# Optimization experiments

Hardware: AMD Instinct MI355X
Metric: run time of the kernel (lower is better)

## Reference

```python
import jax, jax.numpy as jnp
import numpy as np

B, S, D, H = 8, 2048, 1024, 8
HD = D // H


def _linear_params(key, d_in, d_out):
    kw, kb = jax.random.split(key)
    w = jax.random.normal(kw, (d_out, d_in), jnp.float32) * 0.02
    b = jax.random.normal(kb, (d_out,), jnp.float32) * 0.02
    return w, b


def setup_inputs() -> dict:
    key = jax.random.key(0)
    ks = jax.random.split(key, 16)
    inp = {}
    inp['input_seq'] = jax.random.normal(ks[0], (B, S, D), jnp.float32)
    inp['output_seq'] = jax.random.normal(ks[1], (B, S, D), jnp.float32)
    # PositionalEncoding parameter: sin(arange(D) / 10000 ** (arange(D)/D))
    ar = jnp.arange(D, dtype=jnp.float32)
    inp['pe'] = jnp.sin(ar / 10000.0 ** (ar / D))
    names = ['enc_wq enc_bq', 'enc_wk enc_bk', 'enc_wv enc_bv',
             'enc_w1 enc_b1', 'enc_w2 enc_b2',
             'dec_s_wq dec_s_bq', 'dec_s_wk dec_s_bk', 'dec_s_wv dec_s_bv',
             'dec_c_wq dec_c_bq', 'dec_c_wk dec_c_bk', 'dec_c_wv dec_c_bv',
             'dec_w1 dec_b1', 'dec_w2 dec_b2', 'fc_w fc_b']
    for i, pair in enumerate(names):
        wn, bn = pair.split()
        w, b = _linear_params(ks[2 + i], D, D)
        inp[wn], inp[bn] = w, b
    return inp


def _mha(q_in, k_in, wq, bq, wk, bk, wv, bv):
    # Faithful to source: head split WITHOUT transpose -> per-position 8x8 head mixing.
    q = (q_in @ wq.T + bq).reshape(q_in.shape[0], q_in.shape[1], H, HD)
    k = (k_in @ wk.T + bk).reshape(k_in.shape[0], k_in.shape[1], H, HD)
    v = (k_in @ wv.T + bv).reshape(k_in.shape[0], k_in.shape[1], H, HD)
    scores = jnp.einsum('bsih,bsjh->bsij', q, k) / jnp.sqrt(jnp.float32(HD))
    w = jax.nn.softmax(scores, axis=-1)  # dropout before softmax is identity at eval
    out = jnp.einsum('bsij,bsjh->bsih', w, v)
    return out.reshape(q_in.shape[0], q_in.shape[1], -1)


def reference(input_seq, output_seq, pe,
              enc_wq, enc_bq, enc_wk, enc_bk, enc_wv, enc_bv,
              enc_w1, enc_b1, enc_w2, enc_b2,
              dec_s_wq, dec_s_bq, dec_s_wk, dec_s_bk, dec_s_wv, dec_s_bv,
              dec_c_wq, dec_c_bq, dec_c_wk, dec_c_bk, dec_c_wv, dec_c_bv,
              dec_w1, dec_b1, dec_w2, dec_b2, fc_w, fc_b):
    x = input_seq + pe  # additive positional encoding
    # encoder layer
    a = _mha(x, x, enc_wq, enc_bq, enc_wk, enc_bk, enc_wv, enc_bv)
    enc_out = jax.nn.relu(a @ enc_w1.T + enc_b1) @ enc_w2.T + enc_b2
    # decoder layer (training branch: output_seq given)
    sa = _mha(output_seq, output_seq, dec_s_wq, dec_s_bq, dec_s_wk, dec_s_bk, dec_s_wv, dec_s_bv)
    ca = _mha(sa, enc_out, dec_c_wq, dec_c_bq, dec_c_wk, dec_c_bk, dec_c_wv, dec_c_bv)
    dec_out = jax.nn.relu(ca @ dec_w1.T + dec_b1) @ dec_w2.T + dec_b2
    return dec_out @ fc_w.T + fc_b
```

## Files before the change

### kernel.cpp

```cpp
#include <hip/hip_runtime.h>
#include <stdint.h>


#define TOKENS 16384
#define DMODEL 1024

typedef unsigned short ushort_t;
typedef __attribute__((ext_vector_type(8))) short short8;
typedef __attribute__((ext_vector_type(4))) float floatx4;

__device__ __forceinline__ float b2f(ushort_t u) {
  union { uint32_t i; float f; } v; v.i = ((uint32_t)u) << 16; return v.f;
}
__device__ __forceinline__ ushort_t f2b(float f) {
  union { float f; uint32_t i; } v; v.f = f;
  uint32_t r = v.i + 0x7fffu + ((v.i >> 16) & 1u);
  return (ushort_t)(r >> 16);
}

__device__ __forceinline__ void pack8(const float* __restrict__ g, ushort_t* dst) {
  float4 x = *(const float4*)g;
  float4 y = *(const float4*)(g + 4);
  ushort_t o[8] = {f2b(x.x), f2b(x.y), f2b(x.z), f2b(x.w),
                   f2b(y.x), f2b(y.y), f2b(y.z), f2b(y.w)};
  *(uint4*)dst = *(uint4*)o;
}

#define GLD16(g, l)                                                          \
  __builtin_amdgcn_global_load_lds(                                          \
      (const __attribute__((address_space(1))) void*)(g),                    \
      (__attribute__((address_space(3))) void*)(l), 16, 0, 0)

struct ConvArgs {
  const float* src[14];
  ushort_t* dst[14];
};

__global__ __launch_bounds__(256) void conv_w_kernel(ConvArgs a) {
  const int w = blockIdx.y;
  const int idx = (blockIdx.x * 256 + threadIdx.x) * 8;
  pack8(a.src[w] + idx, a.dst[w] + idx);
}

__global__ __launch_bounds__(256) void conv_x_kernel(
    const float* __restrict__ src, ushort_t* __restrict__ dst) {
  const int idx = (blockIdx.x * 256 + threadIdx.x) * 8;
  pack8(src + idx, dst + idx);
}

__global__ __launch_bounds__(256) void add_pe_kernel(
    const float* __restrict__ in, const float* __restrict__ pe,
    ushort_t* __restrict__ out) {
  int idx = (blockIdx.x * 256 + threadIdx.x) * 8;
  int d = idx & (DMODEL - 1);
  float4 a0 = *(const float4*)(in + idx);
  float4 a1 = *(const float4*)(in + idx + 4);
  float4 p0 = *(const float4*)(pe + d);
  float4 p1 = *(const float4*)(pe + d + 4);
  ushort_t o[8] = {f2b(a0.x + p0.x), f2b(a0.y + p0.y), f2b(a0.z + p0.z), f2b(a0.w + p0.w),
                   f2b(a1.x + p1.x), f2b(a1.y + p1.y), f2b(a1.z + p1.z), f2b(a1.w + p1.w)};
  *(uint4*)(out + idx) = *(uint4*)o;
}

template <int D, int MH>
__device__ __forceinline__ void load_a(const ushort_t* sA, int aoff, int cs0,
                                       int cs1, short8 (&af)[4][2]) {
  const ushort_t* p = sA + D * 16384 + MH * 8192 + aoff;
#pragma unroll
  for (int i = 0; i < 4; i++) {
    af[i][0] = *(const short8*)&p[i * 1024 + cs0];
    af[i][1] = *(const short8*)&p[i * 1024 + cs1];
  }
}

template <int D, int NH>
__device__ __forceinline__ void load_b(const ushort_t* sB, int boff, int cs0,
                                       int cs1, short8 (&bf)[2][2]) {
  const ushort_t* p = sB + D * 16384 + NH * 8192 + boff;
#pragma unroll
  for (int j = 0; j < 2; j++) {
    bf[j][0] = *(const short8*)&p[j * 1024 + cs0];
    bf[j][1] = *(const short8*)&p[j * 1024 + cs1];
  }
}

template <int QA, int QB>
__device__ __forceinline__ void mfma_region(floatx4 (&acc)[4][4][2],
                                            const short8 (&af)[4][2],
                                            const short8 (&b0)[2][2],
                                            const short8 (&b1)[2][2]) {
  __builtin_amdgcn_s_setprio(1);
#pragma unroll
  for (int i = 0; i < 4; i++)
#pragma unroll
    for (int j = 0; j < 2; j++) {
      acc[QA][i][j] = __builtin_amdgcn_mfma_f32_16x16x32_bf16(
          af[i][0], b0[j][0], acc[QA][i][j], 0, 0, 0);
      acc[QA][i][j] = __builtin_amdgcn_mfma_f32_16x16x32_bf16(
          af[i][1], b0[j][1], acc[QA][i][j], 0, 0, 0);
    }
#pragma unroll
  for (int i = 0; i < 4; i++)
#pragma unroll
    for (int j = 0; j < 2; j++) {
      acc[QB][i][j] = __builtin_amdgcn_mfma_f32_16x16x32_bf16(
          af[i][0], b1[j][0], acc[QB][i][j], 0, 0, 0);
      acc[QB][i][j] = __builtin_amdgcn_mfma_f32_16x16x32_bf16(
          af[i][1], b1[j][1], acc[QB][i][j], 0, 0, 0);
    }
  __builtin_amdgcn_s_setprio(0);
}

#define BARSB asm volatile("s_barrier" ::: "memory")

#define STAGE_A(h, tk, d)                                                    \
  do {                                                                       \
    GLD16(gA + (size_t)((h) * 131072 + (tk) * 64),                           \
          sA + (d) * 16384 + (h) * 8192 + lo);                               \
    GLD16(gA + (size_t)((h) * 131072 + 65536 + (tk) * 64),                   \
          sA + (d) * 16384 + (h) * 8192 + 4096 + lo);                        \
  } while (0)
#define STAGE_B(h, tk, d)                                                    \
  do {                                                                       \
    GLD16(gB + (size_t)((h) * 131072 + (tk) * 64),                           \
          sB + (d) * 16384 + (h) * 8192 + lo);                               \
    GLD16(gB + (size_t)((h) * 131072 + 65536 + (tk) * 64),                   \
          sB + (d) * 16384 + (h) * 8192 + 4096 + lo);                        \
  } while (0)

#define GROUP(tt, dd)                                                        \
  do {                                                                       \
    load_a<dd, 0>(sA, aoff, cs0, cs1, af);                                   \
    load_b<dd, 0>(sB, boff, cs0, cs1, bf0);                                  \
    load_b<dd, 1>(sB, boff, cs0, cs1, bf1);                                  \
    if ((tt) + 1 < NT) {                                                     \
      STAGE_A(0, (tt) + 1, (dd) ^ 1);                                        \
      STAGE_B(0, (tt) + 1, (dd) ^ 1);                                        \
      STAGE_A(1, (tt) + 1, (dd) ^ 1);                                        \
      STAGE_B(1, (tt) + 1, (dd) ^ 1);                                        \
    }                                                                        \
    mfma_region<0, 1>(acc, af, bf0, bf1);                                    \
    load_a<dd, 1>(sA, aoff, cs0, cs1, af);                                   \
    mfma_region<2, 3>(acc, af, bf0, bf1);                                    \
    asm volatile("s_waitcnt vmcnt(0) lgkmcnt(0)" ::: "memory");              \
    BARSB;                                                                   \
  } while (0)

template <bool RELU, bool OUT32>
__global__ __launch_bounds__(512, 2) void gemm_bt(
    const ushort_t* __restrict__ A, const ushort_t* __restrict__ W,
    const float* __restrict__ bias, void* __restrict__ Cp) {
  constexpr int K = 1024, N = 1024, NT = 16;
  extern __shared__ ushort_t smem[];
  ushort_t* sA = smem;
  ushort_t* sB = smem + 32768;

  const int tid = threadIdx.x;
  const int lane = tid & 63;
  const int wid = tid >> 6;

  const int orig = blockIdx.x;
  const int swz = (orig & 7) * 32 + (orig >> 3);
  const int m0 = (swz >> 2) * 256;
  const int n0 = (swz & 3) * 256;

  const int qm = (wid >> 2) * 64;
  const int qn = (wid & 3) * 32;
  const int lr = lane & 15;
  const int lq = lane >> 4;
  const int xr = lane & 7;
  const int cs0 = (lq ^ xr) * 8;
  const int cs1 = ((4 + lq) ^ xr) * 8;
  const int aoff = (qm + lr) * 64;
  const int boff = (qn + lr) * 64;

  const int rl = tid >> 3;
  const int j8 = tid & 7;
  const int co = (j8 ^ (rl & 7)) * 8;
  const int lo = tid * 8;
  const ushort_t* gA = A + (size_t)(m0 + rl) * K + co;
  const ushort_t* gB = W + (size_t)(n0 + rl) * K + co;

  floatx4 acc[4][4][2] = {};
  short8 af[4][2], bf0[2][2], bf1[2][2];

  STAGE_A(0, 0, 0);
  STAGE_B(0, 0, 0);
  STAGE_A(1, 0, 0);
  STAGE_B(1, 0, 0);
  asm volatile("s_waitcnt vmcnt(0)" ::: "memory");
  BARSB;

#pragma unroll 1
  for (int t = 0; t < NT; t += 2) {
    GROUP(t, 0);
    GROUP(t + 1, 1);
  }

  const int rbase = lq * 4;

  if constexpr (OUT32) {
    float* sCf = (float*)smem;
#pragma unroll
    for (int p = 0; p < 4; p++) {
      if ((qm >> 6) == (p & 1)) {
#pragma unroll
        for (int Nh = 0; Nh < 2; Nh++)
#pragma unroll
          for (int j = 0; j < 2; j++) {
            const int col = Nh * 128 + qn + j * 16 + lr;
            const float bv = bias[n0 + col];
#pragma unroll
            for (int i = 0; i < 4; i++)
#pragma unroll
              for (int r = 0; r < 4; r++) {
                float v = acc[(p >> 1) * 2 + Nh][i][j][r] + bv;
                if (RELU) v = fmaxf(v, 0.0f);
                sCf[(i * 16 + rbase + r) * 260 + col] = v;
              }
          }
      }
      __syncthreads();
#pragma unroll
      for (int u = 0; u < 8; u++) {
        const int lin = u * 512 + tid;
        const int row = lin >> 6;
        const int c4 = (lin & 63) * 4;
        *(float4*)((float*)Cp + (size_t)(m0 + p * 64 + row) * N + n0 + c4) =
            *(const float4*)&sCf[row * 260 + c4];
      }
      __syncthreads();
    }
    return;
  }

  ushort_t* sC = smem;
#pragma unroll
  for (int p = 0; p < 2; p++) {
#pragma unroll
    for (int Nh = 0; Nh < 2; Nh++)
#pragma unroll
      for (int j = 0; j < 2; j++) {
        const int col = Nh * 128 + qn + j * 16 + lr;
        const float bv = bias[n0 + col];
#pragma unroll
        for (int i = 0; i < 4; i++)
#pragma unroll
          for (int r = 0; r < 4; r++) {
            float v = acc[p * 2 + Nh][i][j][r] + bv;
            if (RELU) v = fmaxf(v, 0.0f);
            sC[(qm + i * 16 + rbase + r) * 264 + col] = f2b(v);
          }
      }
    __syncthreads();
#pragma unroll
    for (int u = 0; u < 8; u++) {
      const int lin = u * 512 + tid;
      const int row = lin >> 5;
      const int c8 = (lin & 31) * 8;
      *(uint4*)((ushort_t*)Cp + (size_t)(m0 + p * 128 + row) * N + n0 + c8) =
          *(const uint4*)&sC[row * 264 + c8];
    }
    __syncthreads();
  }
}

__global__ __launch_bounds__(256) void attn_kernel(
    const ushort_t* Q, const ushort_t* Kp, const ushort_t* Vp, ushort_t* O) {
  __shared__ __align__(16) ushort_t sq[4][1024];
  __shared__ __align__(16) ushort_t sk[4][1024];
  __shared__ __align__(16) ushort_t sv[4][1024];
  __shared__ float sp[4][64];

  const int t = threadIdx.x;
  const int w = t >> 6;
  const int lane = t & 63;
  const size_t base = ((size_t)blockIdx.x * 4 + w) * 1024;

  ((uint4*)sq[w])[lane] = ((const uint4*)(Q + base))[lane];
  ((uint4*)sq[w])[lane + 64] = ((const uint4*)(Q + base))[lane + 64];
  ((uint4*)sk[w])[lane] = ((const uint4*)(Kp + base))[lane];
  ((uint4*)sk[w])[lane + 64] = ((const uint4*)(Kp + base))[lane + 64];
  ((uint4*)sv[w])[lane] = ((const uint4*)(Vp + base))[lane];
  ((uint4*)sv[w])[lane + 64] = ((const uint4*)(Vp + base))[lane + 64];
  __syncthreads();

  {
    const int i = lane >> 3, j = lane & 7;
    const ushort_t* qr = &sq[w][i * 128];
    const ushort_t* kr = &sk[w][j * 128];
    float s = 0.0f;
#pragma unroll 16
    for (int h = 0; h < 128; h++) s += b2f(qr[h]) * b2f(kr[h]);
    s *= 0.08838834764831845f;
    float m = s;
#pragma unroll
    for (int off = 1; off < 8; off <<= 1) m = fmaxf(m, __shfl_xor(m, off, 64));
    float e = __expf(s - m);
    float sum = e;
#pragma unroll
    for (int off = 1; off < 8; off <<= 1) sum += __shfl_xor(sum, off, 64);
    sp[w][lane] = e / sum;
  }
  __syncthreads();

  {
    const int i = lane >> 3;
    const int hb = (lane & 7) * 16;
    float p[8];
#pragma unroll
    for (int jj = 0; jj < 8; jj++) p[jj] = sp[w][i * 8 + jj];
    float o[16];
#pragma unroll
    for (int h = 0; h < 16; h++) {
      float acc = 0.0f;
#pragma unroll
      for (int jj = 0; jj < 8; jj++) acc += p[jj] * b2f(sv[w][jj * 128 + hb + h]);
      o[h] = acc;
    }
    uint32_t packed[8];
#pragma unroll
    for (int u = 0; u < 8; u++)
      packed[u] = (uint32_t)f2b(o[2 * u]) | ((uint32_t)f2b(o[2 * u + 1]) << 16);
    uint4* dst = (uint4*)(O + base + i * 128 + hb);
    dst[0] = *(uint4*)&packed[0];
    dst[1] = *(uint4*)&packed[4];
  }
}

extern "C" void kernel_launch(void* const* d_in, const int* in_sizes, int n_in,
                              void* d_out, int out_size, void* d_ws, size_t ws_size,
                              hipStream_t stream) {
  const float* input_seq = (const float*)d_in[0];
  const float* output_seq = (const float*)d_in[1];
  const float* pe = (const float*)d_in[2];
  const float* wsrc[14] = {
      (const float*)d_in[3],  (const float*)d_in[5],  (const float*)d_in[7],
      (const float*)d_in[9],  (const float*)d_in[11], (const float*)d_in[13],
      (const float*)d_in[15], (const float*)d_in[17], (const float*)d_in[19],
      (const float*)d_in[21], (const float*)d_in[23], (const float*)d_in[25],
      (const float*)d_in[27], (const float*)d_in[29]};
  const float* enc_bq = (const float*)d_in[4];
  const float* enc_bk = (const float*)d_in[6];
  const float* enc_bv = (const float*)d_in[8];
  const float* enc_b1 = (const float*)d_in[10];
  const float* enc_b2 = (const float*)d_in[12];
  const float* dsq_b = (const float*)d_in[14];
  const float* dsk_b = (const float*)d_in[16];
  const float* dsv_b = (const float*)d_in[18];
  const float* dcq_b = (const float*)d_in[20];
  const float* dck_b = (const float*)d_in[22];
  const float* dcv_b = (const float*)d_in[24];
  const float* dec_b1 = (const float*)d_in[26];
  const float* dec_b2 = (const float*)d_in[28];
  const float* fc_b = (const float*)d_in[30];

  const size_t SZ = (size_t)TOKENS * DMODEL;
  const size_t WSZ = (size_t)DMODEL * DMODEL;
  ushort_t* bA = (ushort_t*)d_ws;
  ushort_t* bB = bA + SZ;
  ushort_t* oseq = bB + SZ;
  ushort_t* wts = oseq + SZ;
  ushort_t* oL = (ushort_t*)d_out;
  ushort_t* oH = oL + SZ;
  float* outf = (float*)d_out;

  static bool attr_set = false;
  if (!attr_set) {
    (void)hipFuncSetAttribute(reinterpret_cast<const void*>(&gemm_bt<false, false>),
                              hipFuncAttributeMaxDynamicSharedMemorySize, 131072);
    (void)hipFuncSetAttribute(reinterpret_cast<const void*>(&gemm_bt<true, false>),
                              hipFuncAttributeMaxDynamicSharedMemorySize, 131072);
    (void)hipFuncSetAttribute(reinterpret_cast<const void*>(&gemm_bt<false, true>),
                              hipFuncAttributeMaxDynamicSharedMemorySize, 131072);
    attr_set = true;
  }

  ConvArgs ca;
#pragma unroll
  for (int i = 0; i < 14; i++) { ca.src[i] = wsrc[i]; ca.dst[i] = wts + (size_t)i * WSZ; }

  const dim3 gG(TOKENS / 256 * (DMODEL / 256));
  const dim3 gblk(512);
  const dim3 blk(256);
  const int LDSB = 131072;
  const int gPE = TOKENS * DMODEL / (256 * 8);
  const int gAT = TOKENS / 4;

  conv_w_kernel<<<dim3(WSZ / (256 * 8), 14), blk, 0, stream>>>(ca);
  conv_x_kernel<<<gPE, blk, 0, stream>>>(output_seq, oseq);
  add_pe_kernel<<<gPE, blk, 0, stream>>>(input_seq, pe, bA);
  gemm_bt<false, false><<<gG, gblk, LDSB, stream>>>(bA, wts + 0 * WSZ, enc_bq, bB);
  gemm_bt<false, false><<<gG, gblk, LDSB, stream>>>(bA, wts + 1 * WSZ, enc_bk, oL);
  gemm_bt<false, false><<<gG, gblk, LDSB, stream>>>(bA, wts + 2 * WSZ, enc_bv, oH);
  attn_kernel<<<gAT, blk, 0, stream>>>(bB, oL, oH, bB);
  gemm_bt<true, false><<<gG, gblk, LDSB, stream>>>(bB, wts + 3 * WSZ, enc_b1, bA);
  gemm_bt<false, false><<<gG, gblk, LDSB, stream>>>(bA, wts + 4 * WSZ, enc_b2, bB);
  gemm_bt<false, false><<<gG, gblk, LDSB, stream>>>(oseq, wts + 5 * WSZ, dsq_b, bA);
  gemm_bt<false, false><<<gG, gblk, LDSB, stream>>>(oseq, wts + 6 * WSZ, dsk_b, oL);
  gemm_bt<false, false><<<gG, gblk, LDSB, stream>>>(oseq, wts + 7 * WSZ, dsv_b, oH);
  attn_kernel<<<gAT, blk, 0, stream>>>(bA, oL, oH, bA);
  gemm_bt<false, false><<<gG, gblk, LDSB, stream>>>(bA, wts + 8 * WSZ, dcq_b, oL);
  gemm_bt<false, false><<<gG, gblk, LDSB, stream>>>(bB, wts + 9 * WSZ, dck_b, oH);
  gemm_bt<false, false><<<gG, gblk, LDSB, stream>>>(bB, wts + 10 * WSZ, dcv_b, bA);
  attn_kernel<<<gAT, blk, 0, stream>>>(oL, oH, bA, oL);
  gemm_bt<true, false><<<gG, gblk, LDSB, stream>>>(oL, wts + 11 * WSZ, dec_b1, bB);
  gemm_bt<false, false><<<gG, gblk, LDSB, stream>>>(bB, wts + 12 * WSZ, dec_b2, bA);
  gemm_bt<false, true><<<gG, gblk, LDSB, stream>>>(bA, wts + 13 * WSZ, fc_b, outf);
}
```

Measured before the change: 829.6 us.

## Triple-buffer A tiles in GEMM to prefetch two K-steps ahead

Restructures the GEMM main loop so A tiles use a three-slot LDS ring while B stays double-buffered. A is now loaded two K-steps ahead and B one step ahead, and the wait keeps 4 loads outstanding instead of draining every iteration. The goal is to hide global-load latency behind the MFMA work. LDS per block grows from 128KB to 160KB, which lowers blocks per CU from the 2 requested by launch_bounds to 1 and cuts occupancy.

```diff
diff --git a/kernel.cpp b/kernel.cpp
--- a/kernel.cpp
+++ b/kernel.cpp
@@ -62,10 +62,9 @@
   *(uint4*)(out + idx) = *(uint4*)o;
 }
 
-template <int D, int MH>
-__device__ __forceinline__ void load_a(const ushort_t* sA, int aoff, int cs0,
-                                       int cs1, short8 (&af)[4][2]) {
-  const ushort_t* p = sA + D * 16384 + MH * 8192 + aoff;
+__device__ __forceinline__ void load_af(const ushort_t* p, int aoff, int cs0,
+                                        int cs1, short8 (&af)[4][2]) {
+  p += aoff;
 #pragma unroll
   for (int i = 0; i < 4; i++) {
     af[i][0] = *(const short8*)&p[i * 1024 + cs0];
@@ -73,10 +72,9 @@
   }
 }
 
-template <int D, int NH>
-__device__ __forceinline__ void load_b(const ushort_t* sB, int boff, int cs0,
-                                       int cs1, short8 (&bf)[2][2]) {
-  const ushort_t* p = sB + D * 16384 + NH * 8192 + boff;
+__device__ __forceinline__ void load_bf(const ushort_t* p, int boff, int cs0,
+                                        int cs1, short8 (&bf)[2][2]) {
+  p += boff;
 #pragma unroll
   for (int j = 0; j < 2; j++) {
     bf[j][0] = *(const short8*)&p[j * 1024 + cs0];
@@ -113,37 +111,19 @@
 
 #define BARSB asm volatile("s_barrier" ::: "memory")
 
-#define STAGE_A(h, tk, d)                                                    \
+#define STAGE_A4(dst, tk)                                                    \
   do {                                                                       \
-    GLD16(gA + (size_t)((h) * 131072 + (tk) * 64),                           \
-          sA + (d) * 16384 + (h) * 8192 + lo);                               \
-    GLD16(gA + (size_t)((h) * 131072 + 65536 + (tk) * 64),                   \
-          sA + (d) * 16384 + (h) * 8192 + 4096 + lo);                        \
+    GLD16(gA + (size_t)(tk) * 64, (dst) + lo);                               \
+    GLD16(gA + (size_t)(tk) * 64 + 65536, (dst) + 4096 + lo);                \
+    GLD16(gA + (size_t)(tk) * 64 + 131072, (dst) + 8192 + lo);               \
+    GLD16(gA + (size_t)(tk) * 64 + 196608, (dst) + 12288 + lo);              \
   } while (0)
-#define STAGE_B(h, tk, d)                                                    \
+#define STAGE_B4(dst, tk)                                                    \
   do {                                                                       \
-    GLD16(gB + (size_t)((h) * 131072 + (tk) * 64),                           \
-          sB + (d) * 16384 + (h) * 8192 + lo);                               \
-    GLD16(gB + (size_t)((h) * 131072 + 65536 + (tk) * 64),                   \
-          sB + (d) * 16384 + (h) * 8192 + 4096 + lo);                        \
-  } while (0)
-
-#define GROUP(tt, dd)                                                        \
-  do {                                                                       \
-    load_a<dd, 0>(sA, aoff, cs0, cs1, af);                                   \
-    load_b<dd, 0>(sB, boff, cs0, cs1, bf0);                                  \
-    load_b<dd, 1>(sB, boff, cs0, cs1, bf1);                                  \
-    if ((tt) + 1 < NT) {                                                     \
-      STAGE_A(0, (tt) + 1, (dd) ^ 1);                                        \
-      STAGE_B(0, (tt) + 1, (dd) ^ 1);                                        \
-      STAGE_A(1, (tt) + 1, (dd) ^ 1);                                        \
-      STAGE_B(1, (tt) + 1, (dd) ^ 1);                                        \
-    }                                                                        \
-    mfma_region<0, 1>(acc, af, bf0, bf1);                                    \
-    load_a<dd, 1>(sA, aoff, cs0, cs1, af);                                   \
-    mfma_region<2, 3>(acc, af, bf0, bf1);                                    \
-    asm volatile("s_waitcnt vmcnt(0) lgkmcnt(0)" ::: "memory");              \
-    BARSB;                                                                   \
+    GLD16(gB + (size_t)(tk) * 64, (dst) + lo);                               \
+    GLD16(gB + (size_t)(tk) * 64 + 65536, (dst) + 4096 + lo);                \
+    GLD16(gB + (size_t)(tk) * 64 + 131072, (dst) + 8192 + lo);               \
+    GLD16(gB + (size_t)(tk) * 64 + 196608, (dst) + 12288 + lo);              \
   } while (0)
 
 template <bool RELU, bool OUT32>
@@ -153,7 +133,7 @@
   constexpr int K = 1024, N = 1024, NT = 16;
   extern __shared__ ushort_t smem[];
   ushort_t* sA = smem;
-  ushort_t* sB = smem + 32768;
+  ushort_t* sB = smem + 49152;
 
   const int tid = threadIdx.x;
   const int lane = tid & 63;
@@ -184,17 +164,38 @@
   floatx4 acc[4][4][2] = {};
   short8 af[4][2], bf0[2][2], bf1[2][2];
 
-  STAGE_A(0, 0, 0);
-  STAGE_B(0, 0, 0);
-  STAGE_A(1, 0, 0);
-  STAGE_B(1, 0, 0);
-  asm volatile("s_waitcnt vmcnt(0)" ::: "memory");
+  STAGE_A4(sA, 0);
+  STAGE_B4(sB, 0);
+  STAGE_A4(sA + 16384, 1);
+  asm volatile("s_waitcnt vmcnt(4)" ::: "memory");
   BARSB;
 
+  int ba = 0;
 #pragma unroll 1
-  for (int t = 0; t < NT; t += 2) {
-    GROUP(t, 0);
-    GROUP(t + 1, 1);
+  for (int t = 0; t < NT; ++t) {
+    const ushort_t* sAb = sA + ba * 16384;
+    const ushort_t* sBb = sB + (t & 1) * 16384;
+    int ba2 = ba + 2; if (ba2 >= 3) ba2 -= 3;
+    ushort_t* sAs = sA + ba2 * 16384;
+    ushort_t* sBs = sB + ((t + 1) & 1) * 16384;
+
+    if (t + 1 < NT) STAGE_B4(sBs, t + 1);
+    if (t + 2 < NT) STAGE_A4(sAs, t + 2);
+
+    load_af(sAb, aoff, cs0, cs1, af);
+    load_bf(sBb, boff, cs0, cs1, bf0);
+    load_bf(sBb + 8192, boff, cs0, cs1, bf1);
+    mfma_region<0, 1>(acc, af, bf0, bf1);
+    load_af(sAb + 8192, aoff, cs0, cs1, af);
+    mfma_region<2, 3>(acc, af, bf0, bf1);
+
+    if (t + 2 < NT)
+      asm volatile("s_waitcnt vmcnt(4)" ::: "memory");
+    else
+      asm volatile("s_waitcnt vmcnt(0)" ::: "memory");
+    BARSB;
+
+    ba = (ba == 2) ? 0 : ba + 1;
   }
 
   const int rbase = lq * 4;
@@ -368,11 +369,11 @@
   static bool attr_set = false;
   if (!attr_set) {
     (void)hipFuncSetAttribute(reinterpret_cast<const void*>(&gemm_bt<false, false>),
-                              hipFuncAttributeMaxDynamicSharedMemorySize, 131072);
+                              hipFuncAttributeMaxDynamicSharedMemorySize, 163840);
     (void)hipFuncSetAttribute(reinterpret_cast<const void*>(&gemm_bt<true, false>),
-                              hipFuncAttributeMaxDynamicSharedMemorySize, 131072);
+                              hipFuncAttributeMaxDynamicSharedMemorySize, 163840);
     (void)hipFuncSetAttribute(reinterpret_cast<const void*>(&gemm_bt<false, true>),
-                              hipFuncAttributeMaxDynamicSharedMemorySize, 131072);
+                              hipFuncAttributeMaxDynamicSharedMemorySize, 163840);
     attr_set = true;
   }
 
@@ -383,7 +384,7 @@
   const dim3 gG(TOKENS / 256 * (DMODEL / 256));
   const dim3 gblk(512);
   const dim3 blk(256);
-  const int LDSB = 131072;
+  const int LDSB = 163840;
   const int gPE = TOKENS * DMODEL / (256 * 8);
   const int gAT = TOKENS / 4;
 
```

Measured after the change: 845.0 us. About the same (+1.9%).
